# Performance work log

Measured on AMD Instinct MI355X. Metric: run time of the kernel, lower is better.

The kernel has to match this reference:

```python
import jax, jax.numpy as jnp
import numpy as np

N_NODES = 4096
N_EDGES = 16384
D_IN = 128
HID = 1024


def _linear_params(key, fan_in, fan_out):
    kw, kb = jax.random.split(key)
    bound = 1.0 / np.sqrt(fan_in)
    W = jax.random.uniform(kw, (fan_in, fan_out), jnp.float32, -bound, bound)
    b = jax.random.uniform(kb, (fan_out,), jnp.float32, -bound, bound)
    return W, b


def setup_inputs() -> dict:
    key = jax.random.key(0)
    ks = jax.random.split(key, 10)
    H = jax.random.normal(ks[0], (N_NODES, D_IN), jnp.float32)
    e = jax.random.uniform(ks[1], (N_NODES,), jnp.float32)
    # true incidence matrices: one-hot source/destination node per edge
    src = jax.random.randint(ks[2], (N_EDGES,), 0, N_NODES)
    dst = jax.random.randint(ks[3], (N_EDGES,), 0, N_NODES)
    Ro = jax.nn.one_hot(src, N_NODES, dtype=jnp.float32)  # [E, N]
    Ri = jax.nn.one_hot(dst, N_NODES, dtype=jnp.float32)  # [E, N]
    W1, b1 = _linear_params(ks[4], 3 * D_IN, HID)
    W2, b2 = _linear_params(ks[5], HID, HID)
    W3, b3 = _linear_params(ks[6], HID, HID // 2)
    W4, b4 = _linear_params(ks[7], HID // 2, HID // 4)
    W5, b5 = _linear_params(ks[8], HID // 4, 1)
    return {"H": H, "Ro": Ro, "Ri": Ri, "e": e,
            "W1": W1, "b1": b1, "W2": W2, "b2": b2, "W3": W3, "b3": b3,
            "W4": W4, "b4": b4, "W5": W5, "b5": b5}


def reference(H, Ro, Ri, e, W1, b1, W2, b2, W3, b3, W4, b4, W5, b5):
    eH = e[:, None] * H                      # [N, D]
    Ho = Ri.T @ (Ro @ eH)                    # aggregate over edges -> [N, D]
    Hi = Ro.T @ (Ri @ eH)                    # [N, D]
    x = jnp.concatenate([Ho, H, Hi], axis=1)  # [N, 3D]
    x = jnp.tanh(x @ W1 + b1)
    x = jnp.tanh(x @ W2 + b2)
    x = jnp.tanh(x @ W3 + b3)
    x = jnp.tanh(x @ W4 + b4)
    return jax.nn.sigmoid(x @ W5 + b5)       # [N, 1]
```

## Files before the change

kernel.cpp:

```cpp
#include <hip/hip_runtime.h>
#include <hip/hip_bf16.h>
#include <math.h>

#define N_NODES 4096
#define N_EDGES 16384
#define D_IN 128
#define HID 1024

typedef short s8v __attribute__((ext_vector_type(8)));
typedef float f4v __attribute__((ext_vector_type(4)));

__device__ __forceinline__ unsigned short f2b(float v) {
    union { float f; unsigned int u; } c; c.f = v;
    unsigned int u = c.u + 0x7fffu + ((c.u >> 16) & 1u);
    return (unsigned short)(u >> 16);
}
__device__ __forceinline__ float b2f(unsigned short b) {
    union { unsigned int u; float f; } c; c.u = ((unsigned int)b) << 16;
    return c.f;
}
__device__ __forceinline__ void glds16(const unsigned short* g, unsigned short* l) {
    __builtin_amdgcn_global_load_lds(
        (const __attribute__((address_space(1))) void*)g,
        (__attribute__((address_space(3))) void*)l, 16, 0, 0);
}

__global__ void extract_idx(const float* __restrict__ Ro, const float* __restrict__ Ri,
                            int* __restrict__ src, int* __restrict__ dst) {
    __shared__ int found;
    int b = blockIdx.x;
    const float* rowp;
    int* outp;
    if (b < N_EDGES) { rowp = Ro + (size_t)b * N_NODES; outp = src + b; }
    else             { rowp = Ri + (size_t)(b - N_EDGES) * N_NODES; outp = dst + (b - N_EDGES); }
    int t = threadIdx.x;
    if (t == 0) found = 0;
    __syncthreads();
    const float4* r4 = (const float4*)rowp;
    for (int i = 0; i < 4; ++i) {
        int c = t + i * 256;
        float4 v = r4[c];
        if (v.x != 0.0f || v.y != 0.0f || v.z != 0.0f || v.w != 0.0f) {
            int idx = c * 4 + (v.x != 0.0f ? 0 : v.y != 0.0f ? 1 : v.z != 0.0f ? 2 : 3);
            *outp = idx;
            found = 1;
        }
        __syncthreads();
        if (found) break;
    }
}

__global__ void scatter(const int* __restrict__ src, const int* __restrict__ dst,
                        const float* __restrict__ H, const float* __restrict__ e,
                        float* __restrict__ xf) {
    int i = blockIdx.x * 256 + threadIdx.x;
    int ed = i >> 7, j = i & 127;
    int s = src[ed], d = dst[ed];
    atomicAdd(&xf[(size_t)d * 256 + j],       e[s] * H[(size_t)s * 128 + j]);
    atomicAdd(&xf[(size_t)s * 256 + 128 + j], e[d] * H[(size_t)d * 128 + j]);
}

__global__ void cvt_x(const float* __restrict__ xf, const float* __restrict__ H,
                      unsigned short* __restrict__ xb) {
    int n = blockIdx.x, c = threadIdx.x;
    float v;
    if (c < 128)       v = xf[(size_t)n * 256 + c];
    else if (c < 256)  v = H[(size_t)n * 128 + c - 128];
    else               v = xf[(size_t)n * 256 + c - 128];
    xb[(size_t)n * 384 + c] = f2b(v);
}

__global__ void wtrans_all(const float* __restrict__ W1, unsigned short* __restrict__ wt1,
                           const float* __restrict__ W2, unsigned short* __restrict__ wt2,
                           const float* __restrict__ W3, unsigned short* __restrict__ wt3,
                           const float* __restrict__ W4, unsigned short* __restrict__ wt4,
                           const float* __restrict__ W5, unsigned short* __restrict__ wt5) {
    int b = blockIdx.x, t = threadIdx.x;
    const float* W; unsigned short* WT; int K, N, tb;
    if (b < 384)       { W = W1; WT = wt1; K = 384;  N = 1024; tb = b; }
    else if (b < 1408) { W = W2; WT = wt2; K = 1024; N = 1024; tb = b - 384; }
    else if (b < 1920) { W = W3; WT = wt3; K = 1024; N = 512;  tb = b - 1408; }
    else if (b < 2048) { W = W4; WT = wt4; K = 512;  N = 256;  tb = b - 1920; }
    else { wt5[t] = f2b(W5[t]); return; }

    __shared__ float tile[32][33];
    int ntx = N >> 5;
    int tk = tb / ntx, tn = tb - tk * ntx;
    int tr = t >> 5, tc = t & 31;
#pragma unroll
    for (int i = 0; i < 4; ++i)
        tile[tr + i * 8][tc] = W[(size_t)(tk * 32 + tr + i * 8) * N + tn * 32 + tc];
    __syncthreads();
#pragma unroll
    for (int i = 0; i < 4; ++i)
        WT[(size_t)(tn * 32 + tr + i * 8) * K + tk * 32 + tc] = f2b(tile[tc][tr + i * 8]);
}

template<int BM, int BN>
__global__ __launch_bounds__(256)
void gemm_tanh(const unsigned short* __restrict__ A, const unsigned short* __restrict__ BT,
               const float* __restrict__ bias, unsigned short* __restrict__ C,
               int M, int N, int K) {
    constexpr int BK = 32;
    constexpr int MI = BM / 32;
    constexpr int NI = BN / 32;
    constexpr int AITER = BM / 64;
    constexpr int BITER = BN / 64;
    __shared__ unsigned short As[BM * BK];
    __shared__ unsigned short Bs[BN * BK];
    int t = threadIdx.x;
    int l = t & 63, w = t >> 6;
    int wm = w >> 1, wn = w & 1;
    int q = l >> 4, r16 = l & 15;
    int m0 = blockIdx.y * BM, n0 = blockIdx.x * BN;

    f4v acc[MI][NI] = {};

    for (int k0 = 0; k0 < K; k0 += BK) {
        __syncthreads();
#pragma unroll
        for (int i = 0; i < AITER; ++i) {
            int c = (i * 4 + w) * 64 + l;
            int row = c >> 2, ko = (c & 3) * 8;
            glds16(&A[(size_t)(m0 + row) * K + k0 + ko], &As[c * 8]);
        }
#pragma unroll
        for (int i = 0; i < BITER; ++i) {
            int c = (i * 4 + w) * 64 + l;
            int row = c >> 2, ko = (c & 3) * 8;
            glds16(&BT[(size_t)(n0 + row) * K + k0 + ko], &Bs[c * 8]);
        }
        __syncthreads();
        s8v a[MI], b[NI];
#pragma unroll
        for (int mi = 0; mi < MI; ++mi)
            a[mi] = *(const s8v*)&As[(wm * (BM / 2) + mi * 16 + r16) * BK + q * 8];
#pragma unroll
        for (int ni = 0; ni < NI; ++ni)
            b[ni] = *(const s8v*)&Bs[(wn * (BN / 2) + ni * 16 + r16) * BK + q * 8];
#pragma unroll
        for (int mi = 0; mi < MI; ++mi)
#pragma unroll
            for (int ni = 0; ni < NI; ++ni)
                acc[mi][ni] = __builtin_amdgcn_mfma_f32_16x16x32_bf16(a[mi], b[ni], acc[mi][ni], 0, 0, 0);
    }

#pragma unroll
    for (int mi = 0; mi < MI; ++mi) {
#pragma unroll
        for (int ni = 0; ni < NI; ++ni) {
            int col = n0 + wn * (BN / 2) + ni * 16 + r16;
            float bv = bias[col];
#pragma unroll
            for (int r = 0; r < 4; ++r) {
                int row = m0 + wm * (BM / 2) + mi * 16 + q * 4 + r;
                C[(size_t)row * N + col] = f2b(tanhf(acc[mi][ni][r] + bv));
            }
        }
    }
}

__global__ void layer5(const unsigned short* __restrict__ h4, const unsigned short* __restrict__ w5,
                       const float* __restrict__ b5, float* __restrict__ out) {
    int row = blockIdx.x * 4 + (threadIdx.x >> 6);
    int l = threadIdx.x & 63;
    const ushort4 hv = *(const ushort4*)(h4 + (size_t)row * 256 + l * 4);
    const ushort4 wv = *(const ushort4*)(w5 + l * 4);
    float s = b2f(hv.x) * b2f(wv.x) + b2f(hv.y) * b2f(wv.y)
            + b2f(hv.z) * b2f(wv.z) + b2f(hv.w) * b2f(wv.w);
#pragma unroll
    for (int off = 32; off > 0; off >>= 1) s += __shfl_down(s, off);
    if (l == 0) out[row] = 1.0f / (1.0f + expf(-(s + b5[0])));
}

extern "C" void kernel_launch(void* const* d_in, const int* in_sizes, int n_in,
                              void* d_out, int out_size, void* d_ws, size_t ws_size,
                              hipStream_t stream) {
    const float* H  = (const float*)d_in[0];
    const float* Ro = (const float*)d_in[1];
    const float* Ri = (const float*)d_in[2];
    const float* e  = (const float*)d_in[3];
    const float* W1 = (const float*)d_in[4];  const float* b1 = (const float*)d_in[5];
    const float* W2 = (const float*)d_in[6];  const float* b2 = (const float*)d_in[7];
    const float* W3 = (const float*)d_in[8];  const float* b3 = (const float*)d_in[9];
    const float* W4 = (const float*)d_in[10]; const float* b4 = (const float*)d_in[11];
    const float* W5 = (const float*)d_in[12]; const float* b5 = (const float*)d_in[13];
    float* out = (float*)d_out;

    char* p = (char*)d_ws;
    auto alloc = [&](size_t bytes) -> void* {
        void* r = (void*)p;
        p += (bytes + 255) & ~(size_t)255;
        return r;
    };
    int*   src = (int*)  alloc(N_EDGES * 4);
    int*   dst = (int*)  alloc(N_EDGES * 4);
    float* xf  = (float*)alloc((size_t)N_NODES * 256 * 4);
    unsigned short* xb  = (unsigned short*)alloc((size_t)N_NODES * 384 * 2);
    unsigned short* h1  = (unsigned short*)alloc((size_t)N_NODES * HID * 2);
    unsigned short* h2  = (unsigned short*)alloc((size_t)N_NODES * HID * 2);
    unsigned short* h3  = (unsigned short*)alloc((size_t)N_NODES * (HID / 2) * 2);
    unsigned short* h4  = (unsigned short*)alloc((size_t)N_NODES * (HID / 4) * 2);
    unsigned short* wt1 = (unsigned short*)alloc((size_t)HID * 384 * 2);
    unsigned short* wt2 = (unsigned short*)alloc((size_t)HID * HID * 2);
    unsigned short* wt3 = (unsigned short*)alloc((size_t)(HID / 2) * HID * 2);
    unsigned short* wt4 = (unsigned short*)alloc((size_t)(HID / 4) * (HID / 2) * 2);
    unsigned short* wt5 = (unsigned short*)alloc((size_t)(HID / 4) * 2);

    hipMemsetAsync(xf, 0, (size_t)N_NODES * 256 * 4, stream);

    extract_idx<<<2 * N_EDGES, 256, 0, stream>>>(Ro, Ri, src, dst);

    wtrans_all<<<2049, 256, 0, stream>>>(W1, wt1, W2, wt2, W3, wt3, W4, wt4, W5, wt5);

    scatter<<<(N_EDGES * 128) / 256, 256, 0, stream>>>(src, dst, H, e, xf);

    cvt_x<<<N_NODES, 384, 0, stream>>>(xf, H, xb);

    gemm_tanh<128, 64><<<dim3(HID / 64, N_NODES / 128), 256, 0, stream>>>(xb, wt1, b1, h1, N_NODES, HID, 384);
    gemm_tanh<128, 64><<<dim3(HID / 64, N_NODES / 128), 256, 0, stream>>>(h1, wt2, b2, h2, N_NODES, HID, HID);
    gemm_tanh<128, 64><<<dim3((HID / 2) / 64, N_NODES / 128), 256, 0, stream>>>(h2, wt3, b3, h3, N_NODES, HID / 2, HID);
    gemm_tanh<64, 64><<<dim3((HID / 4) / 64, N_NODES / 64), 256, 0, stream>>>(h3, wt4, b4, h4, N_NODES, HID / 4, HID / 2);

    layer5<<<N_NODES / 4, 256, 0, stream>>>(h4, wt5, b5, out);
}
```

Before: 597.3 us.

## Build CSR adjacency for gather aggregation, wave-level index extraction, wider GEMM tiles

Replaces the float atomic scatter plus separate conversion with a pipeline of histogram, prefix scan and CSR fill, followed by a per-node gather that writes the bf16 concatenated input directly. Index extraction now gives each row to one wavefront, using a ballot for early exit instead of a block-wide shared flag with barriers. The first two GEMMs switch to 128x128 tiles. This removes the contended float atomics and the intermediate fp32 buffer, at the cost of extra small kernel launches and a serial scan. Summation order within each node is now fixed, but the CSR list order still depends on atomic ordering.

```diff
diff --git a/kernel.cpp b/kernel.cpp
--- a/kernel.cpp
+++ b/kernel.cpp
@@ -27,47 +27,83 @@
 
 __global__ void extract_idx(const float* __restrict__ Ro, const float* __restrict__ Ri,
                             int* __restrict__ src, int* __restrict__ dst) {
-    __shared__ int found;
-    int b = blockIdx.x;
+    int gw = (blockIdx.x * 256 + threadIdx.x) >> 6;
+    int l = threadIdx.x & 63;
     const float* rowp;
     int* outp;
-    if (b < N_EDGES) { rowp = Ro + (size_t)b * N_NODES; outp = src + b; }
-    else             { rowp = Ri + (size_t)(b - N_EDGES) * N_NODES; outp = dst + (b - N_EDGES); }
+    if (gw < N_EDGES) { rowp = Ro + (size_t)gw * N_NODES; outp = src + gw; }
+    else              { rowp = Ri + (size_t)(gw - N_EDGES) * N_NODES; outp = dst + (gw - N_EDGES); }
+    const float4* r4 = (const float4*)rowp;
+    for (int it = 0; it < 16; ++it) {
+        float4 v = r4[it * 64 + l];
+        bool hit = (v.x != 0.0f) | (v.y != 0.0f) | (v.z != 0.0f) | (v.w != 0.0f);
+        unsigned long long m = __ballot(hit);
+        if (m) {
+            if (hit && l == (__ffsll((long long)m) - 1)) {
+                int base = (it * 64 + l) * 4;
+                *outp = base + (v.x != 0.0f ? 0 : v.y != 0.0f ? 1 : v.z != 0.0f ? 2 : 3);
+            }
+            break;
+        }
+    }
+}
+
+__global__ void hist(const int* __restrict__ src, const int* __restrict__ dst,
+                     int* __restrict__ cnt_o, int* __restrict__ cnt_i) {
+    int e = blockIdx.x * 256 + threadIdx.x;
+    atomicAdd(&cnt_o[dst[e]], 1);
+    atomicAdd(&cnt_i[src[e]], 1);
+}
+
+__global__ __launch_bounds__(1024)
+void scan4096(const int* __restrict__ cnt_o, int* __restrict__ off_o, int* __restrict__ cur_o,
+              const int* __restrict__ cnt_i, int* __restrict__ off_i, int* __restrict__ cur_i) {
+    const int* cnt = blockIdx.x ? cnt_i : cnt_o;
+    int* off = blockIdx.x ? off_i : off_o;
+    int* cur = blockIdx.x ? cur_i : cur_o;
+    __shared__ int part[1024];
     int t = threadIdx.x;
-    if (t == 0) found = 0;
+    int v0 = cnt[t * 4], v1 = cnt[t * 4 + 1], v2 = cnt[t * 4 + 2], v3 = cnt[t * 4 + 3];
+    int sum = v0 + v1 + v2 + v3;
+    part[t] = sum;
     __syncthreads();
-    const float4* r4 = (const float4*)rowp;
-    for (int i = 0; i < 4; ++i) {
-        int c = t + i * 256;
-        float4 v = r4[c];
-        if (v.x != 0.0f || v.y != 0.0f || v.z != 0.0f || v.w != 0.0f) {
-            int idx = c * 4 + (v.x != 0.0f ? 0 : v.y != 0.0f ? 1 : v.z != 0.0f ? 2 : 3);
-            *outp = idx;
-            found = 1;
-        }
-        __syncthreads();
-        if (found) break;
-    }
-}
-
-__global__ void scatter(const int* __restrict__ src, const int* __restrict__ dst,
-                        const float* __restrict__ H, const float* __restrict__ e,
-                        float* __restrict__ xf) {
-    int i = blockIdx.x * 256 + threadIdx.x;
-    int ed = i >> 7, j = i & 127;
-    int s = src[ed], d = dst[ed];
-    atomicAdd(&xf[(size_t)d * 256 + j],       e[s] * H[(size_t)s * 128 + j]);
-    atomicAdd(&xf[(size_t)s * 256 + 128 + j], e[d] * H[(size_t)d * 128 + j]);
-}
-
-__global__ void cvt_x(const float* __restrict__ xf, const float* __restrict__ H,
-                      unsigned short* __restrict__ xb) {
-    int n = blockIdx.x, c = threadIdx.x;
-    float v;
-    if (c < 128)       v = xf[(size_t)n * 256 + c];
-    else if (c < 256)  v = H[(size_t)n * 128 + c - 128];
-    else               v = xf[(size_t)n * 256 + c - 128];
-    xb[(size_t)n * 384 + c] = f2b(v);
+    for (int d = 1; d < 1024; d <<= 1) {
+        int x = (t >= d) ? part[t - d] : 0;
+        __syncthreads();
+        part[t] += x;
+        __syncthreads();
+    }
+    int run = part[t] - sum;
+    off[t * 4] = run;     cur[t * 4] = run;     run += v0;
+    off[t * 4 + 1] = run; cur[t * 4 + 1] = run; run += v1;
+    off[t * 4 + 2] = run; cur[t * 4 + 2] = run; run += v2;
+    off[t * 4 + 3] = run; cur[t * 4 + 3] = run; run += v3;
+    if (t == 1023) off[4096] = run;
+}
+
+__global__ void fill_csr(const int* __restrict__ src, const int* __restrict__ dst,
+                         int* __restrict__ cur_o, int* __restrict__ lst_o,
+                         int* __restrict__ cur_i, int* __restrict__ lst_i) {
+    int e = blockIdx.x * 256 + threadIdx.x;
+    int s = src[e], d = dst[e];
+    lst_o[atomicAdd(&cur_o[d], 1)] = s;
+    lst_i[atomicAdd(&cur_i[s], 1)] = d;
+}
+
+__global__ void aggregate(const int* __restrict__ off_o, const int* __restrict__ lst_o,
+                          const int* __restrict__ off_i, const int* __restrict__ lst_i,
+                          const float* __restrict__ H, const float* __restrict__ e,
+                          unsigned short* __restrict__ xb) {
+    int n = blockIdx.x, f = threadIdx.x;
+    float so = 0.0f, si = 0.0f;
+    int b0 = off_o[n], e0 = off_o[n + 1];
+    for (int k = b0; k < e0; ++k) { int s = lst_o[k]; so += e[s] * H[(size_t)s * 128 + f]; }
+    int b1 = off_i[n], e1 = off_i[n + 1];
+    for (int k = b1; k < e1; ++k) { int d = lst_i[k]; si += e[d] * H[(size_t)d * 128 + f]; }
+    size_t base = (size_t)n * 384;
+    xb[base + f]       = f2b(so);
+    xb[base + 128 + f] = f2b(H[(size_t)n * 128 + f]);
+    xb[base + 256 + f] = f2b(si);
 }
 
 __global__ void wtrans_all(const float* __restrict__ W1, unsigned short* __restrict__ wt1,
@@ -193,9 +229,16 @@
         p += (bytes + 255) & ~(size_t)255;
         return r;
     };
-    int*   src = (int*)  alloc(N_EDGES * 4);
-    int*   dst = (int*)  alloc(N_EDGES * 4);
-    float* xf  = (float*)alloc((size_t)N_NODES * 256 * 4);
+    int* src   = (int*)alloc(N_EDGES * 4);
+    int* dst   = (int*)alloc(N_EDGES * 4);
+    int* cnt_o = (int*)alloc(N_NODES * 4);
+    int* cnt_i = (int*)alloc(N_NODES * 4);
+    int* off_o = (int*)alloc((N_NODES + 1) * 4);
+    int* off_i = (int*)alloc((N_NODES + 1) * 4);
+    int* cur_o = (int*)alloc(N_NODES * 4);
+    int* cur_i = (int*)alloc(N_NODES * 4);
+    int* lst_o = (int*)alloc(N_EDGES * 4);
+    int* lst_i = (int*)alloc(N_EDGES * 4);
     unsigned short* xb  = (unsigned short*)alloc((size_t)N_NODES * 384 * 2);
     unsigned short* h1  = (unsigned short*)alloc((size_t)N_NODES * HID * 2);
     unsigned short* h2  = (unsigned short*)alloc((size_t)N_NODES * HID * 2);
@@ -207,18 +250,20 @@
     unsigned short* wt4 = (unsigned short*)alloc((size_t)(HID / 4) * (HID / 2) * 2);
     unsigned short* wt5 = (unsigned short*)alloc((size_t)(HID / 4) * 2);
 
-    hipMemsetAsync(xf, 0, (size_t)N_NODES * 256 * 4, stream);
-
-    extract_idx<<<2 * N_EDGES, 256, 0, stream>>>(Ro, Ri, src, dst);
+    hipMemsetAsync(cnt_o, 0, 2 * N_NODES * 4, stream);
+
+    extract_idx<<<(2 * N_EDGES) / 4, 256, 0, stream>>>(Ro, Ri, src, dst);
 
     wtrans_all<<<2049, 256, 0, stream>>>(W1, wt1, W2, wt2, W3, wt3, W4, wt4, W5, wt5);
 
-    scatter<<<(N_EDGES * 128) / 256, 256, 0, stream>>>(src, dst, H, e, xf);
-
-    cvt_x<<<N_NODES, 384, 0, stream>>>(xf, H, xb);
-
-    gemm_tanh<128, 64><<<dim3(HID / 64, N_NODES / 128), 256, 0, stream>>>(xb, wt1, b1, h1, N_NODES, HID, 384);
-    gemm_tanh<128, 64><<<dim3(HID / 64, N_NODES / 128), 256, 0, stream>>>(h1, wt2, b2, h2, N_NODES, HID, HID);
+    hist<<<N_EDGES / 256, 256, 0, stream>>>(src, dst, cnt_o, cnt_i);
+    scan4096<<<2, 1024, 0, stream>>>(cnt_o, off_o, cur_o, cnt_i, off_i, cur_i);
+    fill_csr<<<N_EDGES / 256, 256, 0, stream>>>(src, dst, cur_o, lst_o, cur_i, lst_i);
+
+    aggregate<<<N_NODES, 128, 0, stream>>>(off_o, lst_o, off_i, lst_i, H, e, xb);
+
+    gemm_tanh<128, 128><<<dim3(HID / 128, N_NODES / 128), 256, 0, stream>>>(xb, wt1, b1, h1, N_NODES, HID, 384);
+    gemm_tanh<128, 128><<<dim3(HID / 128, N_NODES / 128), 256, 0, stream>>>(h1, wt2, b2, h2, N_NODES, HID, HID);
     gemm_tanh<128, 64><<<dim3((HID / 2) / 64, N_NODES / 128), 256, 0, stream>>>(h2, wt3, b3, h3, N_NODES, HID / 2, HID);
     gemm_tanh<64, 64><<<dim3((HID / 4) / 64, N_NODES / 64), 256, 0, stream>>>(h3, wt4, b4, h4, N_NODES, HID / 4, HID / 2);
 
```

Result: no change. 594.5 us (-0.5%).
